# Performance work log

Hardware: AMD Instinct MI355X
Metric: run time of the kernel (lower is better)

## Reference

```python
import jax, jax.numpy as jnp
import numpy as np

B, D, C = 4096, 1024, 5000
ALPHA, BETA = 1.0, 0.5


def setup_inputs() -> dict:
    key = jax.random.key(0)
    ks = jax.random.split(key, 7)
    return {
        "anchor": jax.random.normal(ks[0], (B, D), dtype=jnp.float32),
        "positive": jax.random.normal(ks[1], (B, D), dtype=jnp.float32),
        "negative": jax.random.normal(ks[2], (B, D), dtype=jnp.float32),
        "outputs": jax.random.normal(ks[3], (3 * B, C), dtype=jnp.float32),
        "labels_anchor": jax.random.randint(ks[4], (B,), 0, C, dtype=jnp.int64),
        "labels_neg": jax.random.randint(ks[5], (B,), 0, C, dtype=jnp.int64),
        "exemplars": jax.random.normal(ks[6], (C, D), dtype=jnp.float32),
    }


def reference(anchor, positive, negative, outputs, labels_anchor, labels_neg, exemplars):
    # Cross-entropy over [3B, C] logits with concatenated labels (mean reduction)
    labels = jnp.concatenate([labels_anchor, labels_anchor, labels_neg], axis=0)
    logp = jax.nn.log_softmax(outputs, axis=-1)
    loss_softmax = -jnp.mean(jnp.take_along_axis(logp, labels[:, None], axis=1))

    # Batched L2 distances anchor -> all exemplars via |a|^2 + |e|^2 - 2 a.e
    a2 = jnp.sum(anchor * anchor, axis=-1, keepdims=True)          # [B,1]
    e2 = jnp.sum(exemplars * exemplars, axis=-1)                   # [C]
    sq = a2 + e2[None, :] - 2.0 * (anchor @ exemplars.T)           # [B,C]
    d_all = jnp.sqrt(jnp.maximum(sq, 0.0))

    d_ref = jnp.take_along_axis(d_all, labels_anchor[:, None], axis=1)[:, 0]  # [B]
    d_closest = jnp.min(d_all, axis=1)                                        # [B]

    tp = jnp.sqrt(jnp.sum((anchor - positive) ** 2, axis=-1))  # [B]
    tn = jnp.sqrt(jnp.sum((anchor - negative) ** 2, axis=-1))  # [B]

    loss_triplet = jnp.sum(jax.nn.relu(tp - tn)).reshape(1)
    loss_center = jnp.sum(jax.nn.relu(d_ref - d_closest)).reshape(1)
    loss_total = loss_softmax + ALPHA * loss_triplet + BETA * loss_center
    return (loss_total, loss_triplet, loss_softmax, loss_center)
```

## Files before the change

kernel.cpp:

```cpp
#include <hip/hip_runtime.h>
#include <hip/hip_bf16.h>

typedef unsigned short u16;
typedef unsigned char u8;
typedef float f32x4 __attribute__((ext_vector_type(4)));
typedef long l2 __attribute__((ext_vector_type(2)));

#define B_ 4096
#define D_ 1024
#define C_ 5000
#define NPAD 5120
#define THREE_B 12288
#define GEMM_BLOCKS 1280
#define CE_BLOCKS 3072

__device__ __forceinline__ float wave_red_sum(float v) {
#pragma unroll
  for (int off = 32; off; off >>= 1) v += __shfl_down(v, off, 64);
  return v;
}

__device__ __forceinline__ void gld_lds16(const u8* g, u8* l) {
  __builtin_amdgcn_global_load_lds(
      (const __attribute__((address_space(1))) unsigned int*)g,
      (__attribute__((address_space(3))) unsigned int*)l, 16, 0, 0);
}

__device__ __forceinline__ int pk_fp8(float4 a) {
  int r = __builtin_amdgcn_cvt_pk_fp8_f32(a.x, a.y, 0, false);
  r = __builtin_amdgcn_cvt_pk_fp8_f32(a.z, a.w, r, true);
  return r;
}

__device__ __forceinline__ int perm_pos(int tid, int r) {
  int kt = tid >> 4;
  int ks = (tid >> 3) & 1;
  int quad = (tid >> 1) & 3;
  int c = quad ^ ((r >> 1) & 3);
  return kt * 64 + c * 16 + ks * 8 + ((tid & 1) << 2);
}

__global__ __launch_bounds__(256) void conv_kernel(
    const float* __restrict__ anchor, const float* __restrict__ positive,
    const float* __restrict__ negative, const float* __restrict__ ex,
    u8* __restrict__ Abf, u8* __restrict__ Ebf, float* __restrict__ a2,
    float* __restrict__ e2, float* __restrict__ trip, float* __restrict__ dmin) {
  int tid = threadIdx.x;
  if (blockIdx.x < B_) {
    int r = blockIdx.x;
    const float4* a4 = (const float4*)(anchor + (size_t)r * D_);
    const float4* p4 = (const float4*)(positive + (size_t)r * D_);
    const float4* n4 = (const float4*)(negative + (size_t)r * D_);
    float4 a = a4[tid], p = p4[tid], n = n4[tid];
    float sa = a.x * a.x + a.y * a.y + a.z * a.z + a.w * a.w;
    float dx = a.x - p.x, dy = a.y - p.y, dz = a.z - p.z, dw = a.w - p.w;
    float sp = dx * dx + dy * dy + dz * dz + dw * dw;
    dx = a.x - n.x; dy = a.y - n.y; dz = a.z - n.z; dw = a.w - n.w;
    float sn = dx * dx + dy * dy + dz * dz + dw * dw;
    *(int*)(Abf + (size_t)r * D_ + perm_pos(tid, r)) = pk_fp8(a);
    __shared__ float red[3][4];
    sa = wave_red_sum(sa); sp = wave_red_sum(sp); sn = wave_red_sum(sn);
    if (!(tid & 63)) { int w = tid >> 6; red[0][w] = sa; red[1][w] = sp; red[2][w] = sn; }
    __syncthreads();
    if (tid == 0) {
      a2[r] = red[0][0] + red[0][1] + red[0][2] + red[0][3];
      float tp = red[1][0] + red[1][1] + red[1][2] + red[1][3];
      float tn = red[2][0] + red[2][1] + red[2][2] + red[2][3];
      trip[r] = fmaxf(sqrtf(tp) - sqrtf(tn), 0.0f);
      dmin[r] = 3.3e38f;
    }
  } else {
    int r = blockIdx.x - B_;
    if (r < C_) {
      const float4* e4 = (const float4*)(ex + (size_t)r * D_);
      float4 e = e4[tid];
      float se = e.x * e.x + e.y * e.y + e.z * e.z + e.w * e.w;
      *(int*)(Ebf + (size_t)r * D_ + perm_pos(tid, r)) = pk_fp8(e);
      __shared__ float red2[4];
      se = wave_red_sum(se);
      if (!(tid & 63)) red2[tid >> 6] = se;
      __syncthreads();
      if (tid == 0) e2[r] = red2[0] + red2[1] + red2[2] + red2[3];
    } else {
      *(int*)(Ebf + (size_t)r * D_ + tid * 4) = 0;
      if (tid == 0) e2[r] = 0.0f;
    }
  }
}

#define BM 128
#define BN 128
#define BKB 64
__global__ __launch_bounds__(256, 3) void gemm_ce_kernel(
    const u8* __restrict__ Abf, const u8* __restrict__ Ebf,
    const float* __restrict__ a2, const float* __restrict__ e2,
    const int* __restrict__ labels, float* __restrict__ dmin,
    float* __restrict__ dref, const float* __restrict__ outputs,
    const int* __restrict__ la, const int* __restrict__ ln,
    float* __restrict__ ce_row) {
  __shared__ alignas(16) u8 As[BM * BKB];
  __shared__ alignas(16) u8 Bs[BN * BKB];
  __shared__ int lab_s[BM];
  __shared__ float a2_s[BM];
  __shared__ float e2_s[BN];

  const int tid = threadIdx.x;

  if (blockIdx.x >= GEMM_BLOCKS) {
    int row_id = ((blockIdx.x - GEMM_BLOCKS) << 2) + (tid >> 6);
    int lane = tid & 63;
    const float* row = outputs + (size_t)row_id * C_;
    const float4* row4 = (const float4*)row;
    const float LOG2E = 1.4426950408889634f;
    float s = 0.0f;
#pragma unroll
    for (int k = 0; k < 19; ++k) {
      float4 v = row4[lane + (k << 6)];
      s += __builtin_amdgcn_exp2f(v.x * LOG2E) + __builtin_amdgcn_exp2f(v.y * LOG2E) +
           __builtin_amdgcn_exp2f(v.z * LOG2E) + __builtin_amdgcn_exp2f(v.w * LOG2E);
    }
    if (lane < 34) {
      float4 v = row4[lane + 19 * 64];
      s += __builtin_amdgcn_exp2f(v.x * LOG2E) + __builtin_amdgcn_exp2f(v.y * LOG2E) +
           __builtin_amdgcn_exp2f(v.z * LOG2E) + __builtin_amdgcn_exp2f(v.w * LOG2E);
    }
    s = wave_red_sum(s);
    if (lane == 0) {
      int label = (row_id < 2 * B_) ? la[row_id & (B_ - 1)] : ln[row_id - 2 * B_];
      ce_row[row_id] = 0.69314718055994531f * __builtin_amdgcn_logf(s) - row[label];
    }
    return;
  }

  const int bm = blockIdx.x & 31;
  const int bn = blockIdx.x >> 5;
  const int lane = tid & 63;
  const int wv = tid >> 6;
  const int wm = wv >> 1, wn = wv & 1;
  const int quad = lane >> 4, l15 = lane & 15;

  if (tid < BM) {
    lab_s[tid] = labels[bm * BM + tid];
    a2_s[tid] = a2[bm * BM + tid];
  } else {
    e2_s[tid - 128] = e2[bn * BN + (tid - 128)];
  }

  f32x4 acc[4][4];
  f32x4 zero4 = {0.0f, 0.0f, 0.0f, 0.0f};
#pragma unroll
  for (int i = 0; i < 4; ++i)
#pragma unroll
    for (int j = 0; j < 4; ++j) acc[i][j] = zero4;

  const u8* Ag = Abf + (size_t)(bm * BM) * D_;
  const u8* Eg = Ebf + (size_t)(bn * BN) * D_;

  for (int k0 = 0; k0 < D_; k0 += BKB) {
    __syncthreads();
#pragma unroll
    for (int t = 0; t < 2; ++t) {
      int id = t * 256 + tid;
      gld_lds16(Ag + (size_t)(id >> 2) * D_ + k0 + (id & 3) * 16, &As[id * 16]);
    }
#pragma unroll
    for (int t = 0; t < 2; ++t) {
      int id = t * 256 + tid;
      gld_lds16(Eg + (size_t)(id >> 2) * D_ + k0 + (id & 3) * 16, &Bs[id * 16]);
    }
    __syncthreads();

    l2 af[4], bfr[4];
#pragma unroll
    for (int i = 0; i < 4; ++i) {
      int r = wm * 64 + i * 16 + l15;
      int c = quad ^ ((r >> 1) & 3);
      af[i] = *(const l2*)&As[r * BKB + c * 16];
    }
#pragma unroll
    for (int j = 0; j < 4; ++j) {
      int r = wn * 64 + j * 16 + l15;
      int c = quad ^ ((r >> 1) & 3);
      bfr[j] = *(const l2*)&Bs[r * BKB + c * 16];
    }
#pragma unroll
    for (int i = 0; i < 4; ++i)
#pragma unroll
      for (int j = 0; j < 4; ++j)
        acc[i][j] = __builtin_amdgcn_mfma_f32_16x16x32_fp8_fp8(
            af[i].x, bfr[j].x, acc[i][j], 0, 0, 0);
#pragma unroll
    for (int i = 0; i < 4; ++i)
#pragma unroll
      for (int j = 0; j < 4; ++j)
        acc[i][j] = __builtin_amdgcn_mfma_f32_16x16x32_fp8_fp8(
            af[i].y, bfr[j].y, acc[i][j], 0, 0, 0);
  }

#pragma unroll
  for (int i = 0; i < 4; ++i) {
    int rbase = wm * 64 + i * 16 + quad * 4;
#pragma unroll
    for (int reg = 0; reg < 4; ++reg) {
      int rloc = rbase + reg;
      int m = bm * BM + rloc;
      float a2m = a2_s[rloc];
      int lab = lab_s[rloc];
      float dmn = 3.0e38f;
#pragma unroll
      for (int j = 0; j < 4; ++j) {
        int nloc = wn * 64 + j * 16 + l15;
        int n = bn * BN + nloc;
        float dot = acc[i][j][reg];
        float sq = a2m + e2_s[nloc] - 2.0f * dot;
        float d = sqrtf(fmaxf(sq, 0.0f));
        if (n < C_) {
          dmn = fminf(dmn, d);
          if (n == lab) dref[m] = d;
        }
      }
#pragma unroll
      for (int msk = 1; msk < 16; msk <<= 1)
        dmn = fminf(dmn, __shfl_xor(dmn, msk, 64));
      if (l15 == 0)
        atomicMin((unsigned int*)&dmin[m], __float_as_uint(dmn));
    }
  }
}

__global__ __launch_bounds__(1024) void final_kernel(
    const float* __restrict__ ce_row, const float* __restrict__ trip,
    const float* __restrict__ dmin, const float* __restrict__ dref,
    float* __restrict__ out) {
  int tid = threadIdx.x;
  float sc = 0.0f, st = 0.0f, sce = 0.0f;
  for (int r = tid; r < B_; r += 1024) {
    sc += fmaxf(dref[r] - dmin[r], 0.0f);
    st += trip[r];
  }
  for (int r = tid; r < THREE_B; r += 1024) sce += ce_row[r];
  __shared__ float red[3][16];
  sc = wave_red_sum(sc); st = wave_red_sum(st); sce = wave_red_sum(sce);
  if (!(tid & 63)) { int w = tid >> 6; red[0][w] = sc; red[1][w] = st; red[2][w] = sce; }
  __syncthreads();
  if (tid == 0) {
    float center = 0.0f, triplet = 0.0f, smx = 0.0f;
#pragma unroll
    for (int w = 0; w < 16; ++w) { center += red[0][w]; triplet += red[1][w]; smx += red[2][w]; }
    float softmax_mean = smx / (float)THREE_B;
    out[0] = softmax_mean + 1.0f * triplet + 0.5f * center;
    out[1] = triplet;
    out[2] = softmax_mean;
    out[3] = center;
  }
}

extern "C" void kernel_launch(void* const* d_in, const int* in_sizes, int n_in,
                              void* d_out, int out_size, void* d_ws, size_t ws_size,
                              hipStream_t stream) {
  const float* anchor = (const float*)d_in[0];
  const float* positive = (const float*)d_in[1];
  const float* negative = (const float*)d_in[2];
  const float* outputs = (const float*)d_in[3];
  const int* la = (const int*)d_in[4];
  const int* ln = (const int*)d_in[5];
  const float* exemplars = (const float*)d_in[6];
  float* out = (float*)d_out;

  float* ws_f = (float*)d_ws;
  float* a2 = ws_f;
  float* e2 = a2 + B_;
  float* dmin = e2 + NPAD;
  float* dref = dmin + B_;
  float* ce_row = dref + B_;
  float* trip = ce_row + THREE_B;
  u8* Abf = (u8*)(trip + B_);
  u8* Ebf = Abf + (size_t)B_ * D_;

  conv_kernel<<<B_ + NPAD, 256, 0, stream>>>(anchor, positive, negative,
                                             exemplars, Abf, Ebf, a2, e2, trip, dmin);
  gemm_ce_kernel<<<GEMM_BLOCKS + CE_BLOCKS, 256, 0, stream>>>(
      Abf, Ebf, a2, e2, la, dmin, dref, outputs, la, ln, ce_row);
  final_kernel<<<1, 1024, 0, stream>>>(ce_row, trip, dmin, dref, out);
}
```

Measured before the change: 411.2 us.

## Use gfx950 16x16x128 scaled FP8 MFMA with 128-byte K tiles

```diff
diff --git a/kernel.cpp b/kernel.cpp
--- a/kernel.cpp
+++ b/kernel.cpp
@@ -4,7 +4,8 @@
 typedef unsigned short u16;
 typedef unsigned char u8;
 typedef float f32x4 __attribute__((ext_vector_type(4)));
-typedef long l2 __attribute__((ext_vector_type(2)));
+typedef int v4i __attribute__((ext_vector_type(4)));
+typedef int v8i __attribute__((ext_vector_type(8)));
 
 #define B_ 4096
 #define D_ 1024
@@ -32,12 +33,10 @@
   return r;
 }
 
-__device__ __forceinline__ int perm_pos(int tid, int r) {
-  int kt = tid >> 4;
-  int ks = (tid >> 3) & 1;
-  int quad = (tid >> 1) & 3;
-  int c = quad ^ ((r >> 1) & 3);
-  return kt * 64 + c * 16 + ks * 8 + ((tid & 1) << 2);
+__device__ __forceinline__ int perm_pos(int t, int r) {
+  int kt = t >> 5;
+  int lc = (t >> 2) & 7;
+  return kt * 128 + ((lc ^ (r & 7)) << 4) + ((t & 3) << 2);
 }
 
 __global__ __launch_bounds__(256) void conv_kernel(
@@ -90,7 +89,7 @@
 
 #define BM 128
 #define BN 128
-#define BKB 64
+#define BKB 128
 __global__ __launch_bounds__(256, 3) void gemm_ce_kernel(
     const u8* __restrict__ Abf, const u8* __restrict__ Ebf,
     const float* __restrict__ a2, const float* __restrict__ e2,
@@ -159,42 +158,40 @@
   for (int k0 = 0; k0 < D_; k0 += BKB) {
     __syncthreads();
 #pragma unroll
-    for (int t = 0; t < 2; ++t) {
+    for (int t = 0; t < 4; ++t) {
       int id = t * 256 + tid;
-      gld_lds16(Ag + (size_t)(id >> 2) * D_ + k0 + (id & 3) * 16, &As[id * 16]);
-    }
-#pragma unroll
-    for (int t = 0; t < 2; ++t) {
+      gld_lds16(Ag + (size_t)(id >> 3) * D_ + k0 + (id & 7) * 16, &As[id * 16]);
+    }
+#pragma unroll
+    for (int t = 0; t < 4; ++t) {
       int id = t * 256 + tid;
-      gld_lds16(Eg + (size_t)(id >> 2) * D_ + k0 + (id & 3) * 16, &Bs[id * 16]);
+      gld_lds16(Eg + (size_t)(id >> 3) * D_ + k0 + (id & 7) * 16, &Bs[id * 16]);
     }
     __syncthreads();
 
-    l2 af[4], bfr[4];
+    v8i af[4], bfr[4];
 #pragma unroll
     for (int i = 0; i < 4; ++i) {
       int r = wm * 64 + i * 16 + l15;
-      int c = quad ^ ((r >> 1) & 3);
-      af[i] = *(const l2*)&As[r * BKB + c * 16];
+      int s = r & 7;
+      v4i lo = *(const v4i*)&As[r * BKB + (((2 * quad) ^ s) << 4)];
+      v4i hi = *(const v4i*)&As[r * BKB + (((2 * quad + 1) ^ s) << 4)];
+      af[i] = __builtin_shufflevector(lo, hi, 0, 1, 2, 3, 4, 5, 6, 7);
     }
 #pragma unroll
     for (int j = 0; j < 4; ++j) {
       int r = wn * 64 + j * 16 + l15;
-      int c = quad ^ ((r >> 1) & 3);
-      bfr[j] = *(const l2*)&Bs[r * BKB + c * 16];
+      int s = r & 7;
+      v4i lo = *(const v4i*)&Bs[r * BKB + (((2 * quad) ^ s) << 4)];
+      v4i hi = *(const v4i*)&Bs[r * BKB + (((2 * quad + 1) ^ s) << 4)];
+      bfr[j] = __builtin_shufflevector(lo, hi, 0, 1, 2, 3, 4, 5, 6, 7);
     }
 #pragma unroll
     for (int i = 0; i < 4; ++i)
 #pragma unroll
       for (int j = 0; j < 4; ++j)
-        acc[i][j] = __builtin_amdgcn_mfma_f32_16x16x32_fp8_fp8(
-            af[i].x, bfr[j].x, acc[i][j], 0, 0, 0);
-#pragma unroll
-    for (int i = 0; i < 4; ++i)
-#pragma unroll
-      for (int j = 0; j < 4; ++j)
-        acc[i][j] = __builtin_amdgcn_mfma_f32_16x16x32_fp8_fp8(
-            af[i].y, bfr[j].y, acc[i][j], 0, 0, 0);
+        acc[i][j] = __builtin_amdgcn_mfma_scale_f32_16x16x128_f8f6f4(
+            af[i], bfr[j], acc[i][j], 0, 0, 0, 127, 0, 127);
   }
 
 #pragma unroll
```

Result: slower. 688.5 us (+67.5%).
